# Kernel optimization log

Measured on AMD Instinct MI355X. Metric: run time of the kernel, lower is better.

## Reference

```python
import jax, jax.numpy as jnp
import numpy as np

C = 128          # hidden channels
N = 40000        # nodes
E = 640000       # edges (avg degree 16)
G = 64           # graphs in batch
STEPS = (5, 4, 3, 2, 1)  # num_layers of each GatedGraphConv


def setup_inputs() -> dict:
    key = jax.random.key(0)
    ks = jax.random.split(key, 9)
    x = jax.random.normal(ks[0], (N, C), jnp.float32)
    edge_index = jax.random.randint(ks[1], (2, E), 0, N, dtype=jnp.int64)
    edge_weights = jax.random.uniform(ks[2], (E,), jnp.float32)
    batch = jnp.sort(jax.random.randint(ks[3], (N,), 0, G, dtype=jnp.int64))
    s = 1.0 / np.sqrt(C)
    # conv_w[k, i] = per-step propagation weight of conv k (unused steps padded)
    conv_w = jax.random.uniform(ks[4], (5, 5, C, C), jnp.float32, -s, s)
    gru_wih = jax.random.uniform(ks[5], (5, 3 * C, C), jnp.float32, -s, s)
    gru_whh = jax.random.uniform(ks[6], (5, 3 * C, C), jnp.float32, -s, s)
    gru_bih = jax.random.uniform(ks[7], (5, 3 * C), jnp.float32, -s, s)
    gru_bhh = jax.random.uniform(ks[8], (5, 3 * C), jnp.float32, -s, s)
    gn_w = jnp.ones((4, C), jnp.float32)
    gn_b = jnp.zeros((4, C), jnp.float32)
    gn_ms = jnp.ones((4, C), jnp.float32)  # GraphNorm mean_scale
    return {"x": x, "edge_weights": edge_weights, "conv_w": conv_w,
            "gru_wih": gru_wih, "gru_whh": gru_whh, "gru_bih": gru_bih,
            "gru_bhh": gru_bhh, "gn_w": gn_w, "gn_b": gn_b, "gn_ms": gn_ms,
            "edge_index": edge_index, "batch": batch}


def _gru(m, h, wih, whh, bih, bhh):
    gi = m @ wih.T + bih
    gh = h @ whh.T + bhh
    ir, iz, inew = jnp.split(gi, 3, axis=-1)
    hr, hz, hn = jnp.split(gh, 3, axis=-1)
    r = jax.nn.sigmoid(ir + hr)
    z = jax.nn.sigmoid(iz + hz)
    n = jnp.tanh(inew + r * hn)
    return (1.0 - z) * n + z * h


def _ggc(x, W, wih, whh, bih, bhh, src, dst, ew, steps):
    # PyG GatedGraphConv: m = x W_i; aggregate sum of ew * m[src] at dst; GRU update.
    for i in range(steps):
        m = x @ W[i]
        msg = m[src]
        if ew is not None:
            msg = msg * ew[:, None]
        agg = jax.ops.segment_sum(msg, dst, num_segments=x.shape[0])
        x = _gru(agg, x, wih, whh, bih, bhh)
    return x


def _graph_norm(x, w, b, ms, eps=1e-5):
    # called with batch=None -> normalize over all nodes as one graph
    mean = jnp.mean(x, axis=0)
    xc = x - ms * mean
    var = jnp.mean(xc * xc, axis=0)
    return w * xc / jnp.sqrt(var + eps) + b


def reference(x, edge_weights, conv_w, gru_wih, gru_whh, gru_bih, gru_bhh,
              gn_w, gn_b, gn_ms, edge_index, batch):
    src, dst = edge_index[0], edge_index[1]
    lrelu = jax.nn.leaky_relu
    o = _ggc(x, conv_w[0], gru_wih[0], gru_whh[0], gru_bih[0], gru_bhh[0], src, dst, edge_weights, STEPS[0])
    o = _graph_norm(o, gn_w[0], gn_b[0], gn_ms[0])
    o = lrelu(o)
    o = _ggc(o, conv_w[1], gru_wih[1], gru_whh[1], gru_bih[1], gru_bhh[1], src, dst, edge_weights, STEPS[1])
    o = lrelu(o)
    o = _graph_norm(o, gn_w[1], gn_b[1], gn_ms[1])
    o = _ggc(o, conv_w[2], gru_wih[2], gru_whh[2], gru_bih[2], gru_bhh[2], src, dst, edge_weights, STEPS[2])
    o = lrelu(o)
    o = _graph_norm(o, gn_w[2], gn_b[2], gn_ms[2])
    o = _ggc(o, conv_w[3], gru_wih[3], gru_whh[3], gru_bih[3], gru_bhh[3], src, dst, edge_weights, STEPS[3])
    o = lrelu(o)
    o = _graph_norm(o, gn_w[3], gn_b[3], gn_ms[3])
    o = _ggc(o, conv_w[4], gru_wih[4], gru_whh[4], gru_bih[4], gru_bhh[4], src, dst, None, STEPS[4])
    o = lrelu(o)
    return jax.ops.segment_sum(o, batch, num_segments=G)
```

## Files before the change

### kernel.cpp

```cpp
#include <hip/hip_runtime.h>
#include <hip/hip_bf16.h>

#define NN 40000
#define EE 640000
#define CCH 128
#define GG 64

typedef __attribute__((ext_vector_type(8))) short short8;
typedef __attribute__((ext_vector_type(4))) float f32x4;

__device__ __forceinline__ float lrelu01(float v){ return v > 0.f ? v : 0.01f*v; }
__device__ __forceinline__ float sigm(float v){ return 1.f/(1.f + __expf(-v)); }
__device__ __forceinline__ float tanh_f(float v){
  v = fminf(fmaxf(v, -15.f), 15.f);
  const float t = __expf(2.f*v);
  return (t - 1.f)/(t + 1.f);
}
__device__ __forceinline__ unsigned short f2bf(float f){
  union { float f; unsigned int u; } v; v.f = f;
  const unsigned int r = v.u + 0x7FFFu + ((v.u >> 16) & 1u);
  return (unsigned short)(r >> 16);
}
__device__ __forceinline__ float bf2f(unsigned short h){
  union { unsigned int u; float f; } v; v.u = ((unsigned int)h) << 16;
  return v.f;
}
__device__ __forceinline__ void split2v(const float4 a, const float4 b, short8& hi, short8& lo){
  const float v[8] = {a.x,a.y,a.z,a.w,b.x,b.y,b.z,b.w};
#pragma unroll
  for (int i=0;i<8;++i){
    const unsigned short h = f2bf(v[i]);
    hi[i] = (short)h;
    lo[i] = (short)f2bf(v[i] - bf2f(h));
  }
}
__device__ __forceinline__ float LDF(const void* p, int f32, size_t i){
  return f32 ? ((const float*)p)[i] : bf2f(((const unsigned short*)p)[i]);
}
__device__ __forceinline__ int LDI(const void* p, int i64, size_t i){
  return i64 ? (int)((const long long*)p)[i] : ((const int*)p)[i];
}

__global__ __launch_bounds__(256) void k_detect(const unsigned short* __restrict__ xh,
                                                const unsigned int* __restrict__ ei,
                                                int* __restrict__ flags){
  __shared__ int s1[256], s2[256];
  const int t = threadIdx.x;
  int c1 = 0, c2 = 0;
  for (int i=0;i<8;++i){
    const unsigned short w = xh[t*8 + i];
    const int e = (w >> 7) & 0xFF;
    if (e < 100 || e > 140) c1++;
    const unsigned int o = ei[(t*8 + i)*2 + 1];
    if (o) c2++;
  }
  s1[t]=c1; s2[t]=c2; __syncthreads();
  for (int off=128; off; off>>=1){ if (t<off){ s1[t]+=s1[t+off]; s2[t]+=s2[t+off]; } __syncthreads(); }
  if (t==0){
    flags[0] = (s1[0] > 64) ? 1 : 0;
    flags[1] = (s2[0] < 16) ? 1 : 0;
  }
}

__global__ __launch_bounds__(256) void k_hist(const void* __restrict__ eidx, const int* __restrict__ flags,
                                              int* __restrict__ deg){
  const int e = blockIdx.x*256 + threadIdx.x;
  if (e >= EE) return;
  atomicAdd(&deg[LDI(eidx, flags[1], (size_t)EE + e)], 1);
}

__global__ __launch_bounds__(256) void k_scan1(const int* __restrict__ deg, int* __restrict__ bsum){
  __shared__ int s[256];
  const int t = threadIdx.x;
  const int i = blockIdx.x*256 + t;
  s[t] = (i < NN) ? deg[i] : 0;
  __syncthreads();
  for (int off=128; off; off>>=1){ if (t<off) s[t]+=s[t+off]; __syncthreads(); }
  if (t==0) bsum[blockIdx.x] = s[0];
}

__global__ __launch_bounds__(256) void k_scan2(const int* __restrict__ bsum, int* __restrict__ boff,
                                               int* __restrict__ roff){
  __shared__ int s[256];
  const int t = threadIdx.x;
  const int v = (t < 157) ? bsum[t] : 0;
  s[t] = v; __syncthreads();
  for (int off=1; off<256; off<<=1){
    const int u = (t>=off) ? s[t-off] : 0;
    __syncthreads(); s[t] += u; __syncthreads();
  }
  if (t < 157) boff[t] = s[t] - v;
  if (t == 0) roff[NN] = EE;
}

__global__ __launch_bounds__(256) void k_scan3(const int* __restrict__ deg, const int* __restrict__ boff,
                                               int* __restrict__ roff, int* __restrict__ pos){
  __shared__ int s[256];
  const int t = threadIdx.x;
  const int i = blockIdx.x*256 + t;
  const int v = (i < NN) ? deg[i] : 0;
  s[t] = v; __syncthreads();
  for (int off=1; off<256; off<<=1){
    const int u = (t>=off) ? s[t-off] : 0;
    __syncthreads(); s[t] += u; __syncthreads();
  }
  if (i < NN){
    const int ex = boff[blockIdx.x] + s[t] - v;
    roff[i] = ex; pos[i] = ex;
  }
}

__global__ __launch_bounds__(256) void k_scatter(const void* __restrict__ eidx, const void* __restrict__ ew,
                                                 const int* __restrict__ flags,
                                                 int* __restrict__ pos, int* __restrict__ es, float* __restrict__ ewt){
  const int e = blockIdx.x*256 + threadIdx.x;
  if (e >= EE) return;
  const int i64 = flags[1];
  const int d = LDI(eidx, i64, (size_t)EE + e);
  const int p = atomicAdd(&pos[d], 1);
  es[p] = LDI(eidx, i64, e);
  ewt[p] = LDF(ew, flags[0], e);
}

__global__ __launch_bounds__(256) void k_x2f(const void* __restrict__ xin, const int* __restrict__ flags,
                                             float* __restrict__ xf){
  const int i = blockIdx.x*256 + threadIdx.x;
  if (i < NN*CCH) xf[i] = LDF(xin, flags[0], i);
}

__global__ __launch_bounds__(256) void k_batcvt(const void* __restrict__ batch, const int* __restrict__ flags,
                                                int* __restrict__ bat32){
  const int i = blockIdx.x*256 + threadIdx.x;
  if (i < NN) bat32[i] = LDI(batch, flags[1], i);
}

__global__ __launch_bounds__(256) void k_wcvt_bf(const void* __restrict__ w, const int* __restrict__ flags,
                                                 const size_t off, unsigned short* __restrict__ o, const int n){
  const int i = blockIdx.x*256 + threadIdx.x;
  if (i < n) o[i] = f2bf(LDF(w, flags[0], off + i));
}

__global__ __launch_bounds__(256) void k_wconvT(const void* __restrict__ w, const int* __restrict__ flags,
                                                const size_t off, unsigned short* __restrict__ o){
  const int i = blockIdx.x*256 + threadIdx.x;
  if (i >= CCH*CCH) return;
  const int c = i >> 7, k = i & 127;
  o[i] = f2bf(LDF(w, flags[0], off + (size_t)k*CCH + c));
}

__global__ __launch_bounds__(256) void k_gemm_m(const float* __restrict__ xf,
                                                const unsigned short* __restrict__ wT,
                                                float* __restrict__ m){
  __shared__ unsigned short s_w[64*128];
  const int tid = threadIdx.x;
  const int wv = tid >> 6;
  const int lane = tid & 63;
  const int quad = lane >> 4;
  const int ln = lane & 15;
  const int bi_ = blockIdx.x >> 1, j = blockIdx.x & 1;
  const int m0 = bi_*64 + wv*16;
  float4 ra[8];
  {
    const float* p = xf + (size_t)(m0 + ln)*CCH + quad*8;
#pragma unroll
    for (int kk=0;kk<4;++kk){
      ra[kk*2]   = *(const float4*)(p + kk*32);
      ra[kk*2+1] = *(const float4*)(p + kk*32 + 4);
    }
  }
  for (int u = tid; u < 1024; u += 256){
    const int c = u >> 4, p = u & 15;
    *(short8*)(s_w + c*128 + ((p ^ (c & 15))*8)) =
      *(const short8*)(wT + (size_t)(j*64 + c)*CCH + p*8);
  }
  short8 fh[4], fl[4];
#pragma unroll
  for (int kk=0;kk<4;++kk) split2v(ra[kk*2], ra[kk*2+1], fh[kk], fl[kk]);
  __syncthreads();
#pragma unroll 1
  for (int ct=0; ct<4; ++ct){
    f32x4 acc = {0.f,0.f,0.f,0.f};
    const int c_local = ct*16 + ln;
#pragma unroll
    for (int kk=0;kk<4;++kk){
      const short8 fb = *(const short8*)(s_w + c_local*128 + (((kk*4+quad) ^ (c_local & 15))*8));
      acc = __builtin_amdgcn_mfma_f32_16x16x32_bf16(fh[kk], fb, acc, 0, 0, 0);
      acc = __builtin_amdgcn_mfma_f32_16x16x32_bf16(fl[kk], fb, acc, 0, 0, 0);
    }
    const int col = j*64 + c_local;
#pragma unroll
    for (int r=0;r<4;++r)
      m[(size_t)(m0 + quad*4 + r)*CCH + col] = acc[r];
  }
}

__global__ __launch_bounds__(256) void k_agg(const float* __restrict__ m, const int* __restrict__ roff,
                                             const int* __restrict__ es, const float* __restrict__ ewt,
                                             float* __restrict__ agg, const int useW){
  const int node = (blockIdx.x*256 + threadIdx.x) >> 6;
  if (node >= NN) return;
  const int lane = threadIdx.x & 63;
  const int h = lane >> 5, j = lane & 31;
  const int beg = roff[node], end = roff[node+1];
  float ax=0.f, ay=0.f, az=0.f, aw=0.f;
  int e = beg + h;
  for (; e + 2 < end; e += 4){
    const int s0 = es[e], s1 = es[e+2];
    const float w0 = useW ? ewt[e] : 1.f;
    const float w1 = useW ? ewt[e+2] : 1.f;
    const float4 v0 = *(const float4*)(m + (size_t)s0*CCH + j*4);
    const float4 v1 = *(const float4*)(m + (size_t)s1*CCH + j*4);
    ax += w0*v0.x + w1*v1.x; ay += w0*v0.y + w1*v1.y;
    az += w0*v0.z + w1*v1.z; aw += w0*v0.w + w1*v1.w;
  }
  if (e < end){
    const int s0 = es[e];
    const float w0 = useW ? ewt[e] : 1.f;
    const float4 v0 = *(const float4*)(m + (size_t)s0*CCH + j*4);
    ax += w0*v0.x; ay += w0*v0.y; az += w0*v0.z; aw += w0*v0.w;
  }
  ax += __shfl_xor(ax, 32); ay += __shfl_xor(ay, 32);
  az += __shfl_xor(az, 32); aw += __shfl_xor(aw, 32);
  if (h == 0){
    float4 ov; ov.x=ax; ov.y=ay; ov.z=az; ov.w=aw;
    *(float4*)(agg + (size_t)node*CCH + j*4) = ov;
  }
}

__global__ __launch_bounds__(256) void k_gru(const float* __restrict__ agg,
                                             float* __restrict__ xf,
                                             const unsigned short* __restrict__ wiB,
                                             const unsigned short* __restrict__ whB,
                                             const void* __restrict__ bih, const void* __restrict__ bhh,
                                             const size_t boff, const int* __restrict__ flags){
  __shared__ unsigned short s_w[6*32*128];
  const int tid = threadIdx.x;
  const int wv = tid >> 6;
  const int lane = tid & 63;
  const int quad = lane >> 4;
  const int ln = lane & 15;
  const int bi_ = blockIdx.x >> 2, j = blockIdx.x & 3;
  const int m0 = bi_*64 + wv*16;
  const int f32 = flags[0];
  float4 ra[8], rx[8];
  {
    const float* pa = agg + (size_t)(m0 + ln)*CCH + quad*8;
    const float* px = xf  + (size_t)(m0 + ln)*CCH + quad*8;
#pragma unroll
    for (int kk=0;kk<4;++kk){
      ra[kk*2]   = *(const float4*)(pa + kk*32);
      ra[kk*2+1] = *(const float4*)(pa + kk*32 + 4);
      rx[kk*2]   = *(const float4*)(px + kk*32);
      rx[kk*2+1] = *(const float4*)(px + kk*32 + 4);
    }
  }
  for (int u = tid; u < 3072; u += 256){
    const int chunk = u >> 9;
    const int rem = u & 511;
    const int c = rem >> 4, p = rem & 15;
    const unsigned short* src = ((chunk < 3) ? wiB : whB)
        + ((size_t)(((chunk<3)?chunk:chunk-3)*CCH + j*32 + c)*CCH + p*8);
    *(short8*)(s_w + chunk*4096 + c*128 + ((p ^ (c & 15))*8)) = *(const short8*)src;
  }
  short8 fah[4], fal[4], fxh[4], fxl[4];
#pragma unroll
  for (int kk=0;kk<4;++kk){
    split2v(ra[kk*2], ra[kk*2+1], fah[kk], fal[kk]);
    split2v(rx[kk*2], rx[kk*2+1], fxh[kk], fxl[kk]);
  }
  __syncthreads();
#pragma unroll 1
  for (int hf=0; hf<2; ++hf){
    const int c_local = hf*16 + ln;
    f32x4 acc[6];
#pragma unroll
    for (int g=0;g<6;++g) acc[g] = (f32x4){0.f,0.f,0.f,0.f};
#pragma unroll
    for (int kk=0;kk<4;++kk){
      const int sw = ((kk*4+quad) ^ (c_local & 15))*8;
#pragma unroll
      for (int g=0;g<3;++g){
        const short8 fbi = *(const short8*)(s_w + g*4096     + c_local*128 + sw);
        const short8 fbh = *(const short8*)(s_w + (3+g)*4096 + c_local*128 + sw);
        acc[g]   = __builtin_amdgcn_mfma_f32_16x16x32_bf16(fah[kk], fbi, acc[g], 0, 0, 0);
        acc[g]   = __builtin_amdgcn_mfma_f32_16x16x32_bf16(fal[kk], fbi, acc[g], 0, 0, 0);
        acc[3+g] = __builtin_amdgcn_mfma_f32_16x16x32_bf16(fxh[kk], fbh, acc[3+g], 0, 0, 0);
        acc[3+g] = __builtin_amdgcn_mfma_f32_16x16x32_bf16(fxl[kk], fbh, acc[3+g], 0, 0, 0);
      }
    }
    const int col = j*32 + c_local;
    float bi[3], bh[3];
#pragma unroll
    for (int g=0;g<3;++g){
      bi[g] = LDF(bih, f32, boff + g*CCH + col);
      bh[g] = LDF(bhh, f32, boff + g*CCH + col);
    }
#pragma unroll
    for (int r=0;r<4;++r){
      const int row = m0 + quad*4 + r;
      const size_t idx = (size_t)row*CCH + col;
      const float h = xf[idx];
      const float rr = sigm(acc[0][r] + acc[3][r] + bi[0] + bh[0]);
      const float zz = sigm(acc[1][r] + acc[4][r] + bi[1] + bh[1]);
      const float nv = tanh_f(acc[2][r] + bi[2] + rr*(acc[5][r] + bh[2]));
      xf[idx] = (1.f - zz)*nv + zz*h;
    }
  }
}

__global__ __launch_bounds__(256) void k_gn_stats(const float* __restrict__ x, float* __restrict__ accum, const int pre){
  const int tid = threadIdx.x;
  const int ch = tid & 127;
  const int half = tid >> 7;
  const int node0 = blockIdx.x * 128;
  float s = 0.f, s2 = 0.f;
  for (int r = half; r < 128; r += 2){
    const int n = node0 + r;
    if (n >= NN) break;
    float v = x[(size_t)n*CCH + ch];
    if (pre) v = lrelu01(v);
    s += v; s2 += v*v;
  }
  __shared__ float buf[256];
  buf[tid] = s; __syncthreads();
  if (tid < 128) atomicAdd(&accum[ch], buf[tid] + buf[tid+128]);
  __syncthreads();
  buf[tid] = s2; __syncthreads();
  if (tid < 128) atomicAdd(&accum[128+ch], buf[tid] + buf[tid+128]);
}

__global__ void k_gn_final(const float* __restrict__ accum, const void* __restrict__ gw,
                           const void* __restrict__ gb, const void* __restrict__ gms,
                           const size_t off, const int* __restrict__ flags, float* __restrict__ par){
  const int j = threadIdx.x;
  const int f32 = flags[0];
  const float inv = 1.f/(float)NN;
  const float mean = accum[j]*inv;
  const float m2 = accum[128+j]*inv;
  const float ms = LDF(gms, f32, off + j);
  const float var = m2 - 2.f*ms*mean*mean + ms*ms*mean*mean;
  const float sc = LDF(gw, f32, off + j) / sqrtf(var + 1e-5f);
  par[j] = sc;
  par[128+j] = LDF(gb, f32, off + j) - sc*ms*mean;
}

__global__ __launch_bounds__(256) void k_gn_apply(float* __restrict__ xf, const float* __restrict__ par, const int mode){
  const int i = blockIdx.x*256 + threadIdx.x;
#pragma unroll
  for (int r=0;r<8;++r){
    const int idx = i + r*640000;
    float v = xf[idx];
    const int ch = idx & 127;
    if (mode == 1) v = lrelu01(v);
    v = par[ch]*v + par[128+ch];
    if (mode == 0) v = lrelu01(v);
    xf[idx] = v;
  }
}

__global__ __launch_bounds__(256) void k_final(const float* __restrict__ x, const int* __restrict__ bat,
                                               float* __restrict__ outf){
  const int t = threadIdx.x;
  const int ch = t & 127;
  const int half = t >> 7;
  const int n0 = blockIdx.x*32;
  int cur = -1; float acc = 0.f;
  for (int r = half; r < 32; r += 2){
    const int n = n0 + r;
    const int b = bat[n];
    if (b != cur){
      if (cur >= 0) atomicAdd(&outf[cur*CCH + ch], acc);
      cur = b; acc = 0.f;
    }
    acc += lrelu01(x[(size_t)n*CCH + ch]);
  }
  if (cur >= 0) atomicAdd(&outf[cur*CCH + ch], acc);
}

__global__ __launch_bounds__(256) void k_store(const float* __restrict__ outf, const int* __restrict__ flags, void* __restrict__ out){
  const int i = blockIdx.x*256 + threadIdx.x;
  if (i >= GG*CCH) return;
  if (flags[0]) ((float*)out)[i] = outf[i];
  else ((unsigned short*)out)[i] = f2bf(outf[i]);
}

extern "C" void kernel_launch(void* const* d_in, const int* in_sizes, int n_in,
                              void* d_out, int out_size, void* d_ws, size_t ws_size,
                              hipStream_t stream){
  const void* x_in = d_in[0];
  const void* ew   = d_in[1];
  const void* cw   = d_in[2];
  const void* wih  = d_in[3];
  const void* whh  = d_in[4];
  const void* bih  = d_in[5];
  const void* bhh  = d_in[6];
  const void* gnw  = d_in[7];
  const void* gnb  = d_in[8];
  const void* gnms = d_in[9];
  const void* eidx  = d_in[10];
  const void* batch = d_in[11];

  float* base = (float*)d_ws;
  size_t o = 0;
  float* xf     = base + o; o += (size_t)NN*CCH;
  float* mbuf   = base + o; o += (size_t)NN*CCH;
  float* aggbuf = base + o; o += (size_t)NN*CCH;
  unsigned short* wconvT= (unsigned short*)(base + o); o += CCH*CCH/2;
  unsigned short* wiB   = (unsigned short*)(base + o); o += 384*CCH/2;
  unsigned short* whB   = (unsigned short*)(base + o); o += 384*CCH/2;
  float* ewt    = base + o; o += EE;
  float* gnpar  = base + o; o += 256;
  int* flags    = (int*)(base + o); o += 2;
  int* bat32    = (int*)(base + o); o += NN;
  int* bsum     = (int*)(base + o); o += 160;
  int* boff2    = (int*)(base + o); o += 160;
  float* outf   = base + o; o += GG*CCH;
  float* gnacc  = base + o; o += 1024;
  int* deg      = (int*)(base + o); o += NN;
  int* roff     = (int*)(base + o); o += NN+1;
  int* pos      = (int*)(base + o); o += NN;
  int* es       = (int*)(base + o); o += EE;

  hipMemsetAsync(outf, 0, (size_t)(GG*CCH + 1024 + NN)*4, stream);

  k_detect<<<1,256,0,stream>>>((const unsigned short*)x_in, (const unsigned int*)eidx, flags);
  k_hist<<<2500,256,0,stream>>>(eidx, flags, deg);
  k_scan1<<<157,256,0,stream>>>(deg, bsum);
  k_scan2<<<1,256,0,stream>>>(bsum, boff2, roff);
  k_scan3<<<157,256,0,stream>>>(deg, boff2, roff, pos);
  k_scatter<<<2500,256,0,stream>>>(eidx, ew, flags, pos, es, ewt);
  k_x2f<<<20000,256,0,stream>>>(x_in, flags, xf);
  k_batcvt<<<157,256,0,stream>>>(batch, flags, bat32);

  const int steps[5] = {5,4,3,2,1};
  for (int L=0; L<5; ++L){
    k_wcvt_bf<<<192,256,0,stream>>>(wih, flags, (size_t)L*384*CCH, wiB, 384*CCH);
    k_wcvt_bf<<<192,256,0,stream>>>(whh, flags, (size_t)L*384*CCH, whB, 384*CCH);
    for (int s=0; s<steps[L]; ++s){
      k_wconvT<<<64,256,0,stream>>>(cw, flags, (size_t)(L*5+s)*CCH*CCH, wconvT);
      k_gemm_m<<<1250,256,0,stream>>>(xf, wconvT, mbuf);
      k_agg<<<10000,256,0,stream>>>(mbuf, roff, es, ewt, aggbuf, (L<4) ? 1 : 0);
      k_gru<<<2500,256,0,stream>>>(aggbuf, xf, wiB, whB, bih, bhh, (size_t)L*384, flags);
    }
    if (L < 4){
      const int pre = (L==0) ? 0 : 1;
      k_gn_stats<<<313,256,0,stream>>>(xf, gnacc + L*256, pre);
      k_gn_final<<<1,128,0,stream>>>(gnacc + L*256, gnw, gnb, gnms, (size_t)L*CCH, flags, gnpar);
      k_gn_apply<<<2500,256,0,stream>>>(xf, gnpar, pre);
    }
  }
  k_final<<<1250,256,0,stream>>>(xf, bat32, outf);
  k_store<<<32,256,0,stream>>>(outf, flags, d_out);
}
```

Baseline: 2.045 ms.

## Fold conv weight into GRU input weight and aggregate raw features

Because aggregation is linear, the step GEMM m = x·W_i is removed: neighbours' x are aggregated directly and then multiplied by a precomputed combined weight W_i·W_ih^T inside the GRU kernel. The combined weights for all 15 steps are built once by a new setup kernel and stored as a bf16 hi/lo pair, and the W_hh conversions are hoisted out of the layer loop. This drops one GEMM kernel and one full N×C intermediate pass per step, and ping-pongs x buffers because the GRU can no longer update in place. In exchange it adds a third MFMA (for the lo part of the weight), a second shared-memory reload phase in the GRU kernel, and a naive scalar product for building the weights.

```diff
diff --git a/kernel.cpp b/kernel.cpp
--- a/kernel.cpp
+++ b/kernel.cpp
@@ -140,57 +140,39 @@
   if (i < n) o[i] = f2bf(LDF(w, flags[0], off + i));
 }
 
-__global__ __launch_bounds__(256) void k_wconvT(const void* __restrict__ w, const int* __restrict__ flags,
-                                                const size_t off, unsigned short* __restrict__ o){
-  const int i = blockIdx.x*256 + threadIdx.x;
-  if (i >= CCH*CCH) return;
-  const int c = i >> 7, k = i & 127;
-  o[i] = f2bf(LDF(w, flags[0], off + (size_t)k*CCH + c));
-}
-
-__global__ __launch_bounds__(256) void k_gemm_m(const float* __restrict__ xf,
-                                                const unsigned short* __restrict__ wT,
-                                                float* __restrict__ m){
-  __shared__ unsigned short s_w[64*128];
+__global__ __launch_bounds__(256) void k_mkWc(const void* __restrict__ cw, const void* __restrict__ wih,
+                                              const int* __restrict__ flags,
+                                              unsigned short* __restrict__ wcH, unsigned short* __restrict__ wcL){
+  __shared__ unsigned short sW[128*128];
+  __shared__ unsigned short sI[32*136];
   const int tid = threadIdx.x;
-  const int wv = tid >> 6;
-  const int lane = tid & 63;
-  const int quad = lane >> 4;
-  const int ln = lane & 15;
-  const int bi_ = blockIdx.x >> 1, j = blockIdx.x & 1;
-  const int m0 = bi_*64 + wv*16;
-  float4 ra[8];
-  {
-    const float* p = xf + (size_t)(m0 + ln)*CCH + quad*8;
-#pragma unroll
-    for (int kk=0;kk<4;++kk){
-      ra[kk*2]   = *(const float4*)(p + kk*32);
-      ra[kk*2+1] = *(const float4*)(p + kk*32 + 4);
-    }
-  }
-  for (int u = tid; u < 1024; u += 256){
-    const int c = u >> 4, p = u & 15;
-    *(short8*)(s_w + c*128 + ((p ^ (c & 15))*8)) =
-      *(const short8*)(wT + (size_t)(j*64 + c)*CCH + p*8);
-  }
-  short8 fh[4], fl[4];
-#pragma unroll
-  for (int kk=0;kk<4;++kk) split2v(ra[kk*2], ra[kk*2+1], fh[kk], fl[kk]);
-  __syncthreads();
-#pragma unroll 1
-  for (int ct=0; ct<4; ++ct){
-    f32x4 acc = {0.f,0.f,0.f,0.f};
-    const int c_local = ct*16 + ln;
-#pragma unroll
-    for (int kk=0;kk<4;++kk){
-      const short8 fb = *(const short8*)(s_w + c_local*128 + (((kk*4+quad) ^ (c_local & 15))*8));
-      acc = __builtin_amdgcn_mfma_f32_16x16x32_bf16(fh[kk], fb, acc, 0, 0, 0);
-      acc = __builtin_amdgcn_mfma_f32_16x16x32_bf16(fl[kk], fb, acc, 0, 0, 0);
-    }
-    const int col = j*64 + c_local;
-#pragma unroll
-    for (int r=0;r<4;++r)
-      m[(size_t)(m0 + quad*4 + r)*CCH + col] = acc[r];
+  const int t = blockIdx.x / 12, tile = blockIdx.x % 12;
+  int L=0, s=t;
+  if (t>=14){L=4;s=t-14;} else if(t>=12){L=3;s=t-12;} else if(t>=9){L=2;s=t-9;} else if(t>=5){L=1;s=t-5;}
+  const int f32 = flags[0];
+  const size_t woff = (size_t)(L*5+s)*16384;
+  const size_t ioff = (size_t)L*49152 + (size_t)tile*32*128;
+  for (int u=tid; u<16384; u+=256) sW[u] = f2bf(LDF(cw, f32, woff + u));
+  for (int u=tid; u<4096; u+=256){
+    const int r = u>>7, jj = u&127;
+    sI[r*136 + jj] = f2bf(LDF(wih, f32, ioff + r*128 + jj));
+  }
+  __syncthreads();
+  const int cl = tid & 31;
+  const int kb = (tid>>5)*16;
+  for (int k=kb; k<kb+16; ++k){
+    float acc = 0.f;
+#pragma unroll 4
+    for (int j8=0; j8<16; ++j8){
+      const short8 a = *(const short8*)(sW + k*128 + j8*8);
+      const short8 b = *(const short8*)(sI + cl*136 + j8*8);
+#pragma unroll
+      for (int q=0;q<8;++q) acc += bf2f((unsigned short)a[q]) * bf2f((unsigned short)b[q]);
+    }
+    const unsigned short h = f2bf(acc);
+    const unsigned short l = f2bf(acc - bf2f(h));
+    const size_t oidx = (size_t)t*49152 + (size_t)(tile*32 + cl)*128 + k;
+    wcH[oidx] = h; wcL[oidx] = l;
   }
 }
 
@@ -227,9 +209,11 @@
   }
 }
 
-__global__ __launch_bounds__(256) void k_gru(const float* __restrict__ agg,
-                                             float* __restrict__ xf,
-                                             const unsigned short* __restrict__ wiB,
+__global__ __launch_bounds__(256) void k_gru(const float* __restrict__ xg,
+                                             const float* __restrict__ xc,
+                                             float* __restrict__ xn,
+                                             const unsigned short* __restrict__ wcH,
+                                             const unsigned short* __restrict__ wcL,
                                              const unsigned short* __restrict__ whB,
                                              const void* __restrict__ bih, const void* __restrict__ bhh,
                                              const size_t boff, const int* __restrict__ flags){
@@ -244,8 +228,8 @@
   const int f32 = flags[0];
   float4 ra[8], rx[8];
   {
-    const float* pa = agg + (size_t)(m0 + ln)*CCH + quad*8;
-    const float* px = xf  + (size_t)(m0 + ln)*CCH + quad*8;
+    const float* pa = xg + (size_t)(m0 + ln)*CCH + quad*8;
+    const float* px = xc + (size_t)(m0 + ln)*CCH + quad*8;
 #pragma unroll
     for (int kk=0;kk<4;++kk){
       ra[kk*2]   = *(const float4*)(pa + kk*32);
@@ -258,8 +242,9 @@
     const int chunk = u >> 9;
     const int rem = u & 511;
     const int c = rem >> 4, p = rem & 15;
-    const unsigned short* src = ((chunk < 3) ? wiB : whB)
-        + ((size_t)(((chunk<3)?chunk:chunk-3)*CCH + j*32 + c)*CCH + p*8);
+    const int gate = (chunk < 3) ? chunk : chunk - 3;
+    const unsigned short* src = ((chunk < 3) ? wcH : wcL)
+        + ((size_t)(gate*CCH + j*32 + c)*CCH + p*8);
     *(short8*)(s_w + chunk*4096 + c*128 + ((p ^ (c & 15))*8)) = *(const short8*)src;
   }
   short8 fah[4], fal[4], fxh[4], fxl[4];
@@ -269,23 +254,48 @@
     split2v(rx[kk*2], rx[kk*2+1], fxh[kk], fxl[kk]);
   }
   __syncthreads();
+  f32x4 acci[2][3];
+#pragma unroll
+  for (int hf=0; hf<2; ++hf){
+    const int c_local = hf*16 + ln;
+#pragma unroll
+    for (int g=0;g<3;++g) acci[hf][g] = (f32x4){0.f,0.f,0.f,0.f};
+#pragma unroll
+    for (int kk=0;kk<4;++kk){
+      const int sw = ((kk*4+quad) ^ (c_local & 15))*8;
+#pragma unroll
+      for (int g=0;g<3;++g){
+        const short8 bh_ = *(const short8*)(s_w + g*4096     + c_local*128 + sw);
+        const short8 bl_ = *(const short8*)(s_w + (3+g)*4096 + c_local*128 + sw);
+        acci[hf][g] = __builtin_amdgcn_mfma_f32_16x16x32_bf16(fah[kk], bh_, acci[hf][g], 0, 0, 0);
+        acci[hf][g] = __builtin_amdgcn_mfma_f32_16x16x32_bf16(fal[kk], bh_, acci[hf][g], 0, 0, 0);
+        acci[hf][g] = __builtin_amdgcn_mfma_f32_16x16x32_bf16(fah[kk], bl_, acci[hf][g], 0, 0, 0);
+      }
+    }
+  }
+  __syncthreads();
+  for (int u = tid; u < 1536; u += 256){
+    const int chunk = u >> 9;
+    const int rem = u & 511;
+    const int c = rem >> 4, p = rem & 15;
+    const unsigned short* src = whB + ((size_t)(chunk*CCH + j*32 + c)*CCH + p*8);
+    *(short8*)(s_w + chunk*4096 + c*128 + ((p ^ (c & 15))*8)) = *(const short8*)src;
+  }
+  __syncthreads();
 #pragma unroll 1
   for (int hf=0; hf<2; ++hf){
     const int c_local = hf*16 + ln;
-    f32x4 acc[6];
-#pragma unroll
-    for (int g=0;g<6;++g) acc[g] = (f32x4){0.f,0.f,0.f,0.f};
+    f32x4 acch[3];
+#pragma unroll
+    for (int g=0;g<3;++g) acch[g] = (f32x4){0.f,0.f,0.f,0.f};
 #pragma unroll
     for (int kk=0;kk<4;++kk){
       const int sw = ((kk*4+quad) ^ (c_local & 15))*8;
 #pragma unroll
       for (int g=0;g<3;++g){
-        const short8 fbi = *(const short8*)(s_w + g*4096     + c_local*128 + sw);
-        const short8 fbh = *(const short8*)(s_w + (3+g)*4096 + c_local*128 + sw);
-        acc[g]   = __builtin_amdgcn_mfma_f32_16x16x32_bf16(fah[kk], fbi, acc[g], 0, 0, 0);
-        acc[g]   = __builtin_amdgcn_mfma_f32_16x16x32_bf16(fal[kk], fbi, acc[g], 0, 0, 0);
-        acc[3+g] = __builtin_amdgcn_mfma_f32_16x16x32_bf16(fxh[kk], fbh, acc[3+g], 0, 0, 0);
-        acc[3+g] = __builtin_amdgcn_mfma_f32_16x16x32_bf16(fxl[kk], fbh, acc[3+g], 0, 0, 0);
+        const short8 bh_ = *(const short8*)(s_w + g*4096 + c_local*128 + sw);
+        acch[g] = __builtin_amdgcn_mfma_f32_16x16x32_bf16(fxh[kk], bh_, acch[g], 0, 0, 0);
+        acch[g] = __builtin_amdgcn_mfma_f32_16x16x32_bf16(fxl[kk], bh_, acch[g], 0, 0, 0);
       }
     }
     const int col = j*32 + c_local;
@@ -299,11 +309,11 @@
     for (int r=0;r<4;++r){
       const int row = m0 + quad*4 + r;
       const size_t idx = (size_t)row*CCH + col;
-      const float h = xf[idx];
-      const float rr = sigm(acc[0][r] + acc[3][r] + bi[0] + bh[0]);
-      const float zz = sigm(acc[1][r] + acc[4][r] + bi[1] + bh[1]);
-      const float nv = tanh_f(acc[2][r] + bi[2] + rr*(acc[5][r] + bh[2]));
-      xf[idx] = (1.f - zz)*nv + zz*h;
+      const float h = xc[idx];
+      const float rr = sigm(acci[hf][0][r] + acch[0][r] + bi[0] + bh[0]);
+      const float zz = sigm(acci[hf][1][r] + acch[1][r] + bi[1] + bh[1]);
+      const float nv = tanh_f(acci[hf][2][r] + bi[2] + rr*(acch[2][r] + bh[2]));
+      xn[idx] = (1.f - zz)*nv + zz*h;
     }
   }
 }
@@ -402,12 +412,12 @@
 
   float* base = (float*)d_ws;
   size_t o = 0;
-  float* xf     = base + o; o += (size_t)NN*CCH;
-  float* mbuf   = base + o; o += (size_t)NN*CCH;
-  float* aggbuf = base + o; o += (size_t)NN*CCH;
-  unsigned short* wconvT= (unsigned short*)(base + o); o += CCH*CCH/2;
-  unsigned short* wiB   = (unsigned short*)(base + o); o += 384*CCH/2;
-  unsigned short* whB   = (unsigned short*)(base + o); o += 384*CCH/2;
+  float* xA     = base + o; o += (size_t)NN*CCH;
+  float* xB     = base + o; o += (size_t)NN*CCH;
+  float* xg     = base + o; o += (size_t)NN*CCH;
+  unsigned short* wcH = (unsigned short*)(base + o); o += 15*384*CCH/2;
+  unsigned short* wcL = (unsigned short*)(base + o); o += 15*384*CCH/2;
+  unsigned short* whB5= (unsigned short*)(base + o); o += 5*384*CCH/2;
   float* ewt    = base + o; o += EE;
   float* gnpar  = base + o; o += 256;
   int* flags    = (int*)(base + o); o += 2;
@@ -429,26 +439,32 @@
   k_scan2<<<1,256,0,stream>>>(bsum, boff2, roff);
   k_scan3<<<157,256,0,stream>>>(deg, boff2, roff, pos);
   k_scatter<<<2500,256,0,stream>>>(eidx, ew, flags, pos, es, ewt);
-  k_x2f<<<20000,256,0,stream>>>(x_in, flags, xf);
+  k_x2f<<<20000,256,0,stream>>>(x_in, flags, xA);
   k_batcvt<<<157,256,0,stream>>>(batch, flags, bat32);
+  for (int L=0; L<5; ++L)
+    k_wcvt_bf<<<192,256,0,stream>>>(whh, flags, (size_t)L*384*CCH, whB5 + (size_t)L*384*CCH, 384*CCH);
+  k_mkWc<<<180,256,0,stream>>>(cw, wih, flags, wcH, wcL);
 
   const int steps[5] = {5,4,3,2,1};
+  float* xc = xA;
+  float* xn = xB;
+  int t = 0;
   for (int L=0; L<5; ++L){
-    k_wcvt_bf<<<192,256,0,stream>>>(wih, flags, (size_t)L*384*CCH, wiB, 384*CCH);
-    k_wcvt_bf<<<192,256,0,stream>>>(whh, flags, (size_t)L*384*CCH, whB, 384*CCH);
     for (int s=0; s<steps[L]; ++s){
-      k_wconvT<<<64,256,0,stream>>>(cw, flags, (size_t)(L*5+s)*CCH*CCH, wconvT);
-      k_gemm_m<<<1250,256,0,stream>>>(xf, wconvT, mbuf);
-      k_agg<<<10000,256,0,stream>>>(mbuf, roff, es, ewt, aggbuf, (L<4) ? 1 : 0);
-      k_gru<<<2500,256,0,stream>>>(aggbuf, xf, wiB, whB, bih, bhh, (size_t)L*384, flags);
+      k_agg<<<10000,256,0,stream>>>(xc, roff, es, ewt, xg, (L<4) ? 1 : 0);
+      k_gru<<<2500,256,0,stream>>>(xg, xc, xn,
+                                   wcH + (size_t)t*384*CCH, wcL + (size_t)t*384*CCH,
+                                   whB5 + (size_t)L*384*CCH, bih, bhh, (size_t)L*384, flags);
+      float* tmp = xc; xc = xn; xn = tmp;
+      t++;
     }
     if (L < 4){
       const int pre = (L==0) ? 0 : 1;
-      k_gn_stats<<<313,256,0,stream>>>(xf, gnacc + L*256, pre);
+      k_gn_stats<<<313,256,0,stream>>>(xc, gnacc + L*256, pre);
       k_gn_final<<<1,128,0,stream>>>(gnacc + L*256, gnw, gnb, gnms, (size_t)L*CCH, flags, gnpar);
-      k_gn_apply<<<2500,256,0,stream>>>(xf, gnpar, pre);
-    }
-  }
-  k_final<<<1250,256,0,stream>>>(xf, bat32, outf);
+      k_gn_apply<<<2500,256,0,stream>>>(xc, gnpar, pre);
+    }
+  }
+  k_final<<<1250,256,0,stream>>>(xc, bat32, outf);
   k_store<<<32,256,0,stream>>>(outf, flags, d_out);
 }
```

Measured after the change: 2.113 ms. 3.3% more time.
